# Kernel tuning notes

Hardware: AMD Instinct MI355X
Metric: run time of the kernel (lower is better)

The kernel has to match this reference:

```python
import jax, jax.numpy as jnp
import numpy as np

N_NODES = 50000
N_EDGES = 800000
IN_F, HID_F, OUT_F = 256, 128, 64


def setup_inputs() -> dict:
    key = jax.random.key(0)
    ks = jax.random.split(key, 9)
    glorot = lambda k, shp: jax.random.normal(k, shp, jnp.float32) * np.sqrt(2.0 / (shp[0] + shp[1]))
    return {
        "x": jax.random.normal(ks[0], (N_NODES, IN_F), jnp.float32),
        "W1": glorot(ks[1], (IN_F, HID_F)),
        "b1": jnp.zeros((HID_F,), jnp.float32),
        "W2": glorot(ks[2], (HID_F, OUT_F)),
        "b2": jnp.zeros((OUT_F,), jnp.float32),
        "Wf": glorot(ks[3], (OUT_F, 2)),
        "bf": jnp.zeros((2,), jnp.float32),
        "src": jax.random.randint(ks[4], (N_EDGES,), 0, N_NODES, jnp.int32),
        "dst": jax.random.randint(ks[5], (N_EDGES,), 0, N_NODES, jnp.int32),
    }


def _gcn_layer(x, src, dst, W, b):
    # DGL GraphConv, norm='both': h = D_in^{-1/2} A D_out^{-1/2} (x W) + b
    n = x.shape[0]
    ones = jnp.ones((src.shape[0],), x.dtype)
    deg_out = jnp.clip(jax.ops.segment_sum(ones, src, num_segments=n), 1.0)
    deg_in = jnp.clip(jax.ops.segment_sum(ones, dst, num_segments=n), 1.0)
    h = x @ W  # transform first (in_feats >= out_feats), cheaper messages
    h = h * jax.lax.rsqrt(deg_out)[:, None]
    agg = jax.ops.segment_sum(h[src], dst, num_segments=n)  # [N, F] sparse aggregate
    return agg * jax.lax.rsqrt(deg_in)[:, None] + b


def reference(x, W1, b1, W2, b2, Wf, bf, src, dst):
    h1 = jax.nn.relu(_gcn_layer(x, src, dst, W1, b1))
    hidden = _gcn_layer(h1, src, dst, W2, b2)
    logits = hidden @ Wf + bf
    return (logits, hidden)
```

## Files before the change

kernel.cpp:

```cpp
#include <hip/hip_runtime.h>
#include <hip/hip_bf16.h>
#include <cstdint>
#include <cstddef>

#define NNODES 50000
#define NEDGES 800000
#define NCH    256
#define CHUNK1 3125
#define NBUCK  196
#define GB1    782
#define SHB    64
#define SHE    12500
#define SHEV   (SHE / 1024)
#define PBN    256
#define PBR    196

typedef unsigned short u16;
typedef unsigned int u32;
typedef short bfrag8 __attribute__((ext_vector_type(8)));
typedef float f32x4 __attribute__((ext_vector_type(4)));

__device__ __forceinline__ u16 f2bf(float f) {
    union { float f; uint32_t i; } v; v.f = f;
    uint32_t r = (v.i + 0x7FFFu + ((v.i >> 16) & 1u)) >> 16;
    return (u16)r;
}
__device__ __forceinline__ float bflo(u32 p) { union { uint32_t i; float f; } v; v.i = p << 16; return v.f; }
__device__ __forceinline__ float bfhi(u32 p) { union { uint32_t i; float f; } v; v.i = p & 0xFFFF0000u; return v.f; }

__global__ __launch_bounds__(256) void pre_kernel(const float* __restrict__ W1, const float* __restrict__ W2,
                                                  u16* __restrict__ P1, u16* __restrict__ P2,
                                                  const int* __restrict__ src, const int* __restrict__ dst,
                                                  u32* __restrict__ histS, u32* __restrict__ histD,
                                                  u32* __restrict__ gh1, int nE) {
    __shared__ u32 hh[12500];
    int b = blockIdx.x, t = threadIdx.x;
    if (b < 2 * SHB) {
        const int* col = (b < SHB) ? src : dst;
        int bb = (b < SHB) ? b : b - SHB;
        for (int j = t; j < 12500; j += 256) hh[j] = 0;
        __syncthreads();
        int beg = bb * SHE;
        const uint4* col4 = (const uint4*)(col + beg);
        #pragma unroll 4
        for (int k = 0; k < SHEV; k++) {
            uint4 e = col4[k * 256 + t];
            atomicAdd(&hh[e.x >> 2], 1u << ((e.x & 3) * 8));
            atomicAdd(&hh[e.y >> 2], 1u << ((e.y & 3) * 8));
            atomicAdd(&hh[e.z >> 2], 1u << ((e.z & 3) * 8));
            atomicAdd(&hh[e.w >> 2], 1u << ((e.w & 3) * 8));
        }
        for (int i = beg + SHEV * 1024 + t; i < beg + SHE; i += 256) {
            u32 n = (u32)col[i];
            atomicAdd(&hh[n >> 2], 1u << ((n & 3) * 8));
        }
        __syncthreads();
        u32* out = ((b < SHB) ? histS : histD) + (size_t)bb * 12500;
        for (int j = t; j < 12500; j += 256) out[j] = hh[j];
    } else if (b < 2 * SHB + NCH) {
        int c = b - 2 * SHB;
        hh[t] = 0;
        __syncthreads();
        int beg = c * CHUNK1, end = min(beg + CHUNK1, nE);
        for (int i = beg + t; i < end; i += 256)
            atomicAdd(&hh[(u32)dst[i] >> 8], 1u);
        __syncthreads();
        gh1[t * NCH + c] = hh[t];
    } else {
        int i = (b - 2 * SHB - NCH) * 256 + t;
        if (i < 256 * 128) {
            int k = i >> 7, n = i & 127;
            P1[((((k >> 3) << 7) + n) << 3) | (k & 7)] = f2bf(W1[i]);
        }
        if (i < 128 * 64) {
            int k = i >> 6, n = i & 63;
            P2[((((k >> 3) << 6) + n) << 3) | (k & 7)] = f2bf(W2[i]);
        }
    }
}

__global__ __launch_bounds__(256) void red_scan1(const u32* __restrict__ histS, const u32* __restrict__ histD,
                                                 int* __restrict__ deg_out, int* __restrict__ deg_in,
                                                 const u32* __restrict__ gh1, int* __restrict__ scan1,
                                                 int* __restrict__ part1, int* __restrict__ gdh) {
    int t = threadIdx.x, b = blockIdx.x;
    __shared__ int sd[256];
    __shared__ int cnt64[64];
    if (t < 64) cnt64[t] = 0;
    int gi = b * NCH + t;
    int v = (int)gh1[gi];
    sd[t] = v;
    __syncthreads();
    #pragma unroll
    for (int o = 1; o < 256; o <<= 1) {
        int add = (t >= o) ? sd[t - o] : 0;
        __syncthreads();
        sd[t] += add;
        __syncthreads();
    }
    scan1[gi] = sd[t];
    if (t == 255) part1[b] = sd[255];
    int n = b * PBR + t;
    if (t < PBR && n < NNODES) {
        int w = n >> 2, sh = (n & 3) * 8;
        int so = 0, si = 0;
        #pragma unroll 8
        for (int r = 0; r < SHB; r++) {
            so += (int)((histS[(size_t)r * 12500 + w] >> sh) & 255u);
            si += (int)((histD[(size_t)r * 12500 + w] >> sh) & 255u);
        }
        deg_out[n] = so;
        deg_in[n] = si;
        atomicAdd(&cnt64[si > 63 ? 63 : si], 1);
    }
    __syncthreads();
    if (t < 64) gdh[b * 64 + t] = cnt64[t];
}

__global__ __launch_bounds__(256) void scatter1(const int* __restrict__ dst, const int* __restrict__ src,
                                                const u32* __restrict__ gh1, const int* __restrict__ scan1,
                                                const int* __restrict__ part1, u32* __restrict__ sbuf,
                                                const int* __restrict__ gdh, int* __restrict__ gbase, int nE) {
    int t = threadIdx.x, c = blockIdx.x;
    if (c == NCH) {
        __shared__ int colsum[64];
        if (t < 64) {
            int s = 0;
            for (int pb = 0; pb < PBN; pb++) s += gdh[pb * 64 + t];
            colsum[t] = s;
        }
        __syncthreads();
        if (t == 0) {
            int s = 0;
            for (int d = 0; d < 64; d++) { int c0 = colsum[d]; colsum[d] = s; s += c0; }
        }
        __syncthreads();
        if (t < 64) {
            int s = colsum[t];
            for (int pb = 0; pb < PBN; pb++) { gbase[pb * 64 + t] = s; s += gdh[pb * 64 + t]; }
        }
        return;
    }
    __shared__ int sd[256];
    __shared__ int offs[256];
    __shared__ u32 base[256];
    __shared__ u32 lh[256];
    int v = part1[t];
    sd[t] = v;
    __syncthreads();
    #pragma unroll
    for (int o = 1; o < 256; o <<= 1) {
        int add = (t >= o) ? sd[t - o] : 0;
        __syncthreads();
        sd[t] += add;
        __syncthreads();
    }
    offs[t] = sd[t] - v;
    __syncthreads();
    base[t] = (u32)(scan1[t * NCH + c] + offs[t] - (int)gh1[t * NCH + c]);
    lh[t] = 0;
    __syncthreads();
    int beg = c * CHUNK1, end = min(beg + CHUNK1, nE);
    for (int i = beg + t; i < end; i += 256) {
        u32 el = ((u32)dst[i] << 16) | (u32)src[i];
        u32 d = el >> 24;
        u32 r = atomicAdd(&lh[d], 1);
        sbuf[base[d] + r] = el;
    }
}

template <int K, int N, bool AF32>
__device__ __forceinline__ void gemm_body(const void* __restrict__ A_, const u16* __restrict__ Wp,
                                          const int* __restrict__ deg, u16* __restrict__ out, int M, int bx) {
    const int lane = threadIdx.x & 63;
    const int wave = threadIdx.x >> 6;
    const int m = lane & 15;
    const int q = lane >> 4;
    const int row0 = bx * 64 + wave * 16;

    int rowa = row0 + m; if (rowa > M - 1) rowa = M - 1;

    constexpr int NT = N / 16;
    f32x4 acc[NT];
    #pragma unroll
    for (int t = 0; t < NT; t++) acc[t] = (f32x4){0.f, 0.f, 0.f, 0.f};

    #pragma unroll
    for (int kc = 0; kc < K; kc += 32) {
        bfrag8 af;
        if constexpr (AF32) {
            const float* ap = (const float*)A_ + (size_t)rowa * K + q * 8 + kc;
            const float4 x0 = *(const float4*)(ap);
            const float4 x1 = *(const float4*)(ap + 4);
            af[0] = (short)f2bf(x0.x); af[1] = (short)f2bf(x0.y);
            af[2] = (short)f2bf(x0.z); af[3] = (short)f2bf(x0.w);
            af[4] = (short)f2bf(x1.x); af[5] = (short)f2bf(x1.y);
            af[6] = (short)f2bf(x1.z); af[7] = (short)f2bf(x1.w);
        } else {
            const u16* ap = (const u16*)A_ + (size_t)rowa * K + q * 8 + kc;
            af = *(const bfrag8*)ap;
        }
        const u16* bbase = Wp + ((size_t)(((kc >> 3) + q) * N) + m) * 8;
        #pragma unroll
        for (int t = 0; t < NT; t++) {
            bfrag8 bf_ = *(const bfrag8*)(bbase + t * 128);
            acc[t] = __builtin_amdgcn_mfma_f32_16x16x32_bf16(af, bf_, acc[t], 0, 0, 0);
        }
    }
    #pragma unroll
    for (int r = 0; r < 4; r++) {
        int gr = row0 + q * 4 + r;
        if (gr < M) {
            int dO = deg[gr]; if (dO < 1) dO = 1;
            float s = rsqrtf((float)dO);
            #pragma unroll
            for (int t = 0; t < NT; t++)
                out[(size_t)gr * N + t * 16 + m] = f2bf(acc[t][r] * s);
        }
    }
}

template <int K, int N, bool AF32>
__global__ __launch_bounds__(256) void gemm_scaled(const void* __restrict__ A_, const u16* __restrict__ Wp,
                                                   const int* __restrict__ deg, u16* __restrict__ out, int M) {
    gemm_body<K, N, AF32>(A_, Wp, deg, out, M, blockIdx.x);
}

__global__ __launch_bounds__(256) void sort_gemm(const u32* __restrict__ sbuf, const int* __restrict__ part1,
                                                 u32* __restrict__ sorted, int* __restrict__ rp,
                                                 const float* __restrict__ x, const u16* __restrict__ Wp1,
                                                 const int* __restrict__ deg_out, const int* __restrict__ deg_in,
                                                 const int* __restrict__ gbase, int* __restrict__ perm,
                                                 u16* __restrict__ h, int nE) {
    int b = blockIdx.x, t = threadIdx.x;
    if (b < NBUCK) {
        __shared__ int sd[256];
        __shared__ int cnt[256];
        __shared__ int cursor[256];
        int v = part1[t];
        sd[t] = v;
        __syncthreads();
        #pragma unroll
        for (int o = 1; o < 256; o <<= 1) {
            int add = (t >= o) ? sd[t - o] : 0;
            __syncthreads();
            sd[t] += add;
            __syncthreads();
        }
        __shared__ int bs_s, bl_s;
        if (t == b) { bs_s = sd[t] - v; bl_s = v; }
        __syncthreads();
        int bstart = bs_s, bend = bstart + bl_s;
        cnt[t] = 0;
        __syncthreads();
        for (int i = bstart + t; i < bend; i += 256)
            atomicAdd(&cnt[(sbuf[i] >> 16) & 255u], 1);
        __syncthreads();
        int cv = cnt[t];
        sd[t] = cv;
        __syncthreads();
        #pragma unroll
        for (int o = 1; o < 256; o <<= 1) {
            int add = (t >= o) ? sd[t - o] : 0;
            __syncthreads();
            sd[t] += add;
            __syncthreads();
        }
        int excl = sd[t] - cv;
        int node = b * 256 + t;
        if (node < NNODES) rp[node] = bstart + excl;
        if (b == NBUCK - 1 && t == 0) rp[NNODES] = nE;
        cursor[t] = excl;
        __syncthreads();
        for (int i = bstart + t; i < bend; i += 256) {
            u32 el = sbuf[i];
            int r = atomicAdd(&cursor[(el >> 16) & 255u], 1);
            sorted[bstart + r] = el;
        }
    } else if (b < NBUCK + GB1) {
        gemm_body<256, 128, true>(x, Wp1, deg_out, h, NNODES, b - NBUCK);
    } else {
        int pb = b - NBUCK - GB1;
        __shared__ int cur[64];
        if (t < 64) cur[t] = gbase[pb * 64 + t];
        __syncthreads();
        int n = pb * PBR + t;
        if (t < PBR && n < NNODES) {
            int d = deg_in[n]; d = d > 63 ? 63 : d;
            int p = atomicAdd(&cur[d], 1);
            perm[p] = n;
        }
    }
}

__global__ __launch_bounds__(256) void gather1(const uint4* __restrict__ h, const int* __restrict__ row_ptr,
                                               const u32* __restrict__ sorted, const float* __restrict__ b1,
                                               const int* __restrict__ perm,
                                               uint4* __restrict__ h1out, int nNodes) {
    int g = (blockIdx.x * 256 + threadIdx.x) >> 4;
    int l = threadIdx.x & 15;
    if (g >= nNodes) return;
    int node = perm[g];
    int beg = row_ptr[node], end = row_ptr[node + 1];
    float a[8] = {0.f, 0.f, 0.f, 0.f, 0.f, 0.f, 0.f, 0.f};
    for (int e = beg; e < end; e += 8) {
        uint4 p[8];
        #pragma unroll
        for (int j = 0; j < 8; j++) {
            int ee = e + j; ee = (ee < end - 1) ? ee : end - 1;
            p[j] = h[(size_t)(sorted[ee] & 0xFFFFu) * 16 + l];
        }
        #pragma unroll
        for (int j = 0; j < 8; j++)
            if (e + j < end) {
                a[0] += bflo(p[j].x); a[1] += bfhi(p[j].x);
                a[2] += bflo(p[j].y); a[3] += bfhi(p[j].y);
                a[4] += bflo(p[j].z); a[5] += bfhi(p[j].z);
                a[6] += bflo(p[j].w); a[7] += bfhi(p[j].w);
            }
    }
    int dI = end - beg; if (dI < 1) dI = 1;
    float r = rsqrtf((float)dI);
    const float4 bA = *(const float4*)(b1 + 8 * l);
    const float4 bB = *(const float4*)(b1 + 8 * l + 4);
    float v0 = fmaxf(a[0] * r + bA.x, 0.f), v1 = fmaxf(a[1] * r + bA.y, 0.f);
    float v2 = fmaxf(a[2] * r + bA.z, 0.f), v3 = fmaxf(a[3] * r + bA.w, 0.f);
    float v4 = fmaxf(a[4] * r + bB.x, 0.f), v5 = fmaxf(a[5] * r + bB.y, 0.f);
    float v6 = fmaxf(a[6] * r + bB.z, 0.f), v7 = fmaxf(a[7] * r + bB.w, 0.f);
    uint4 o;
    o.x = ((u32)f2bf(v1) << 16) | f2bf(v0);
    o.y = ((u32)f2bf(v3) << 16) | f2bf(v2);
    o.z = ((u32)f2bf(v5) << 16) | f2bf(v4);
    o.w = ((u32)f2bf(v7) << 16) | f2bf(v6);
    h1out[(size_t)node * 16 + l] = o;
}

__global__ __launch_bounds__(256) void gather2(const uint4* __restrict__ h2, const int* __restrict__ row_ptr,
                                               const u32* __restrict__ sorted, const float* __restrict__ b2,
                                               const float* __restrict__ Wf, const float* __restrict__ bfv,
                                               const int* __restrict__ perm,
                                               float* __restrict__ logits, float* __restrict__ hidden, int nNodes) {
    int g = (blockIdx.x * 256 + threadIdx.x) >> 3;
    int l = threadIdx.x & 7;
    if (g >= nNodes) return;
    int node = perm[g];
    int beg = row_ptr[node], end = row_ptr[node + 1];
    float a[8] = {0.f, 0.f, 0.f, 0.f, 0.f, 0.f, 0.f, 0.f};
    for (int e = beg; e < end; e += 8) {
        uint4 p[8];
        #pragma unroll
        for (int j = 0; j < 8; j++) {
            int ee = e + j; ee = (ee < end - 1) ? ee : end - 1;
            p[j] = h2[(size_t)(sorted[ee] & 0xFFFFu) * 8 + l];
        }
        #pragma unroll
        for (int j = 0; j < 8; j++)
            if (e + j < end) {
                a[0] += bflo(p[j].x); a[1] += bfhi(p[j].x);
                a[2] += bflo(p[j].y); a[3] += bfhi(p[j].y);
                a[4] += bflo(p[j].z); a[5] += bfhi(p[j].z);
                a[6] += bflo(p[j].w); a[7] += bfhi(p[j].w);
            }
    }
    int dI = end - beg; if (dI < 1) dI = 1;
    float r = rsqrtf((float)dI);
    float v[8];
    #pragma unroll
    for (int f = 0; f < 8; f++) v[f] = a[f] * r + b2[8 * l + f];
    float4 oA = {v[0], v[1], v[2], v[3]};
    float4 oB = {v[4], v[5], v[6], v[7]};
    ((float4*)hidden)[(size_t)node * 16 + 2 * l + 0] = oA;
    ((float4*)hidden)[(size_t)node * 16 + 2 * l + 1] = oB;
    float l0 = 0.f, l1 = 0.f;
    #pragma unroll
    for (int f = 0; f < 8; f++) {
        l0 += v[f] * Wf[(8 * l + f) * 2 + 0];
        l1 += v[f] * Wf[(8 * l + f) * 2 + 1];
    }
    #pragma unroll
    for (int off = 4; off > 0; off >>= 1) {
        l0 += __shfl_down(l0, off, 8);
        l1 += __shfl_down(l1, off, 8);
    }
    if (l == 0) {
        logits[(size_t)node * 2 + 0] = l0 + bfv[0];
        logits[(size_t)node * 2 + 1] = l1 + bfv[1];
    }
}

extern "C" void kernel_launch(void* const* d_in, const int* in_sizes, int n_in,
                              void* d_out, int out_size, void* d_ws, size_t ws_size,
                              hipStream_t stream) {
    const float* x   = (const float*)d_in[0];
    const float* W1  = (const float*)d_in[1];
    const float* b1  = (const float*)d_in[2];
    const float* W2  = (const float*)d_in[3];
    const float* b2  = (const float*)d_in[4];
    const float* Wf  = (const float*)d_in[5];
    const float* bfv = (const float*)d_in[6];
    const int* src = (const int*)d_in[7];
    const int* dst = (const int*)d_in[8];

    float* out_logits = (float*)d_out;
    float* out_hidden = (float*)d_out + 2 * NNODES;

    char* ws = (char*)d_ws;
    size_t off = 0;
    auto alloc = [&](size_t bytes) { void* p = ws + off; off += (bytes + 255) & ~(size_t)255; return p; };
    u32*   gh1     = (u32*)alloc(NCH * NCH * 4);
    int*   scan1   = (int*)alloc(NCH * NCH * 4);
    int*   part1   = (int*)alloc(256 * 4);
    u32*   sbuf    = (u32*)alloc((size_t)NEDGES * 4);
    u32*   sorted  = (u32*)alloc((size_t)NEDGES * 4);
    u32*   histS   = (u32*)alloc((size_t)SHB * 12500 * 4);
    u32*   histD   = (u32*)alloc((size_t)SHB * 12500 * 4);
    int*   deg     = (int*)alloc(2 * NNODES * 4);
    int*   row_ptr = (int*)alloc((NNODES + 1) * 4);
    int*   gdh     = (int*)alloc(PBN * 64 * 4);
    int*   gbase   = (int*)alloc(PBN * 64 * 4);
    int*   perm    = (int*)alloc(NNODES * 4);
    u16*   Wp1     = (u16*)alloc(256 * 128 * 2);
    u16*   Wp2     = (u16*)alloc(128 * 64 * 2);
    u16*   h       = (u16*)alloc((size_t)NNODES * 128 * 2);
    u16*   h1      = (u16*)alloc((size_t)NNODES * 128 * 2);
    u16*   h2      = (u16*)alloc((size_t)NNODES * 64 * 2);

    int* deg_out = deg;
    int* deg_in  = deg + NNODES;

    pre_kernel<<<2 * SHB + NCH + 128, 256, 0, stream>>>(W1, W2, Wp1, Wp2, src, dst, histS, histD, gh1, NEDGES);
    red_scan1<<<NCH, 256, 0, stream>>>(histS, histD, deg_out, deg_in, gh1, scan1, part1, gdh);
    scatter1<<<NCH + 1, 256, 0, stream>>>(dst, src, gh1, scan1, part1, sbuf, gdh, gbase, NEDGES);
    sort_gemm<<<NBUCK + GB1 + PBN, 256, 0, stream>>>(sbuf, part1, sorted, row_ptr, x, Wp1,
                                                     deg_out, deg_in, gbase, perm, h, NEDGES);
    gather1<<<(NNODES * 16) / 256, 256, 0, stream>>>((const uint4*)h, row_ptr, sorted, b1, perm,
                                                     (uint4*)h1, NNODES);
    gemm_scaled<128, 64, false><<<GB1, 256, 0, stream>>>(h1, Wp2, deg_out, h2, NNODES);
    gather2<<<(NNODES * 8 + 255) / 256, 256, 0, stream>>>((const uint4*)h2, row_ptr, sorted, b2, Wf, bfv,
                                                          perm, out_logits, out_hidden, NNODES);
}
```

Before: 202.9 us.

## Fuse layer-1 aggregation with layer-2 GEMM and vectorize edge-index loads

The first-layer gather kernel now stages each block's 16 aggregated, ReLU'd node rows in shared memory. It then multiplies them directly by W2 using MFMA and writes the deg_out-scaled h2. This removes the separate gemm_scaled launch and the round trip of the 50000x128 h1 buffer through global memory. The histogram and scatter loops also read src/dst as uint4, with CHUNK1 changed so chunk boundaries are multiples of four. The risks are an extra block-wide barrier inside the gather kernel and small per-block MFMA work that may leave the matrix units underused.

After: 195.8 us. -3.5%, faster.

```diff
diff --git a/kernel.cpp b/kernel.cpp
--- a/kernel.cpp
+++ b/kernel.cpp
@@ -6,7 +6,7 @@
 #define NNODES 50000
 #define NEDGES 800000
 #define NCH    256
-#define CHUNK1 3125
+#define CHUNK1 3136
 #define NBUCK  196
 #define GB1    782
 #define SHB    64
@@ -62,8 +62,15 @@
         hh[t] = 0;
         __syncthreads();
         int beg = c * CHUNK1, end = min(beg + CHUNK1, nE);
-        for (int i = beg + t; i < end; i += 256)
-            atomicAdd(&hh[(u32)dst[i] >> 8], 1u);
+        const uint4* d4 = (const uint4*)(dst + beg);
+        int n4 = (end - beg) >> 2;
+        for (int k = t; k < n4; k += 256) {
+            uint4 e = d4[k];
+            atomicAdd(&hh[e.x >> 8], 1u);
+            atomicAdd(&hh[e.y >> 8], 1u);
+            atomicAdd(&hh[e.z >> 8], 1u);
+            atomicAdd(&hh[e.w >> 8], 1u);
+        }
         __syncthreads();
         gh1[t * NCH + c] = hh[t];
     } else {
@@ -161,11 +168,16 @@
     lh[t] = 0;
     __syncthreads();
     int beg = c * CHUNK1, end = min(beg + CHUNK1, nE);
-    for (int i = beg + t; i < end; i += 256) {
-        u32 el = ((u32)dst[i] << 16) | (u32)src[i];
-        u32 d = el >> 24;
-        u32 r = atomicAdd(&lh[d], 1);
-        sbuf[base[d] + r] = el;
+    const uint4* s4 = (const uint4*)(src + beg);
+    const uint4* d4 = (const uint4*)(dst + beg);
+    int n4 = (end - beg) >> 2;
+    for (int k = t; k < n4; k += 256) {
+        uint4 es = s4[k], ed = d4[k];
+        u32 el, dg, r;
+        el = (ed.x << 16) | es.x; dg = el >> 24; r = atomicAdd(&lh[dg], 1); sbuf[base[dg] + r] = el;
+        el = (ed.y << 16) | es.y; dg = el >> 24; r = atomicAdd(&lh[dg], 1); sbuf[base[dg] + r] = el;
+        el = (ed.z << 16) | es.z; dg = el >> 24; r = atomicAdd(&lh[dg], 1); sbuf[base[dg] + r] = el;
+        el = (ed.w << 16) | es.w; dg = el >> 24; r = atomicAdd(&lh[dg], 1); sbuf[base[dg] + r] = el;
     }
 }
 
@@ -293,13 +305,15 @@
     }
 }
 
-__global__ __launch_bounds__(256) void gather1(const uint4* __restrict__ h, const int* __restrict__ row_ptr,
-                                               const u32* __restrict__ sorted, const float* __restrict__ b1,
-                                               const int* __restrict__ perm,
-                                               uint4* __restrict__ h1out, int nNodes) {
-    int g = (blockIdx.x * 256 + threadIdx.x) >> 4;
-    int l = threadIdx.x & 15;
-    if (g >= nNodes) return;
+__global__ __launch_bounds__(256) void gather1f(const uint4* __restrict__ h, const int* __restrict__ row_ptr,
+                                                const u32* __restrict__ sorted, const float* __restrict__ b1,
+                                                const int* __restrict__ perm, const int* __restrict__ deg_out,
+                                                const u16* __restrict__ Wp2, u16* __restrict__ h2) {
+    __shared__ __align__(16) u16 sh[16 * 136];
+    int t = threadIdx.x;
+    int qw = t >> 4;
+    int l = t & 15;
+    int g = blockIdx.x * 16 + qw;
     int node = perm[g];
     int beg = row_ptr[node], end = row_ptr[node + 1];
     float a[8] = {0.f, 0.f, 0.f, 0.f, 0.f, 0.f, 0.f, 0.f};
@@ -332,7 +346,27 @@
     o.y = ((u32)f2bf(v3) << 16) | f2bf(v2);
     o.z = ((u32)f2bf(v5) << 16) | f2bf(v4);
     o.w = ((u32)f2bf(v7) << 16) | f2bf(v6);
-    h1out[(size_t)node * 16 + l] = o;
+    *(uint4*)&sh[qw * 136 + l * 8] = o;
+    __syncthreads();
+    const int lane = t & 63;
+    const int m = lane & 15;
+    const int q = lane >> 4;
+    const int w = t >> 6;
+    f32x4 acc = (f32x4){0.f, 0.f, 0.f, 0.f};
+    #pragma unroll
+    for (int kc = 0; kc < 128; kc += 32) {
+        bfrag8 af = *(const bfrag8*)&sh[m * 136 + q * 8 + kc];
+        bfrag8 bf_ = *(const bfrag8*)(Wp2 + ((size_t)(((kc >> 3) + q) * 64) + w * 16 + m) * 8);
+        acc = __builtin_amdgcn_mfma_f32_16x16x32_bf16(af, bf_, acc, 0, 0, 0);
+    }
+    #pragma unroll
+    for (int rr = 0; rr < 4; rr++) {
+        int li = q * 4 + rr;
+        int nd = perm[blockIdx.x * 16 + li];
+        int dO = deg_out[nd]; if (dO < 1) dO = 1;
+        float s = rsqrtf((float)dO);
+        h2[(size_t)nd * 64 + w * 16 + m] = f2bf(acc[rr] * s);
+    }
 }
 
 __global__ __launch_bounds__(256) void gather2(const uint4* __restrict__ h2, const int* __restrict__ row_ptr,
@@ -422,7 +456,6 @@
     u16*   Wp1     = (u16*)alloc(256 * 128 * 2);
     u16*   Wp2     = (u16*)alloc(128 * 64 * 2);
     u16*   h       = (u16*)alloc((size_t)NNODES * 128 * 2);
-    u16*   h1      = (u16*)alloc((size_t)NNODES * 128 * 2);
     u16*   h2      = (u16*)alloc((size_t)NNODES * 64 * 2);
 
     int* deg_out = deg;
@@ -433,9 +466,7 @@
     scatter1<<<NCH + 1, 256, 0, stream>>>(dst, src, gh1, scan1, part1, sbuf, gdh, gbase, NEDGES);
     sort_gemm<<<NBUCK + GB1 + PBN, 256, 0, stream>>>(sbuf, part1, sorted, row_ptr, x, Wp1,
                                                      deg_out, deg_in, gbase, perm, h, NEDGES);
-    gather1<<<(NNODES * 16) / 256, 256, 0, stream>>>((const uint4*)h, row_ptr, sorted, b1, perm,
-                                                     (uint4*)h1, NNODES);
-    gemm_scaled<128, 64, false><<<GB1, 256, 0, stream>>>(h1, Wp2, deg_out, h2, NNODES);
+    gather1f<<<NNODES / 16, 256, 0, stream>>>((const uint4*)h, row_ptr, sorted, b1, perm, deg_out, Wp2, h2);
     gather2<<<(NNODES * 8 + 255) / 256, 256, 0, stream>>>((const uint4*)h2, row_ptr, sorted, b2, Wf, bfv,
                                                           perm, out_logits, out_hidden, NNODES);
 }
```
